# Optimization experiments

Hardware: AMD Instinct MI355X
Metric: run time of the kernel (lower is better)

Reference implementation:

```python
import jax, jax.numpy as jnp
import numpy as np


def setup_inputs() -> dict:
    key = jax.random.key(0)
    k1, k2, k3 = jax.random.split(key, 3)
    x = jax.random.normal(k1, (8, 2048, 512), dtype=jnp.float32)
    codebook = jax.random.normal(k2, (8192, 512), dtype=jnp.float32)
    values = jax.random.normal(k3, (8192, 512), dtype=jnp.float32)
    return {"x": x, "codebook": codebook, "values": values}


def reference(x, codebook, values):
    # VectorQuantize: nearest codebook entry under squared L2 distance.
    # dist(b,n,k) = ||x_bn||^2 - 2 x_bn . e_k + ||e_k||^2
    x_sq = jnp.sum(x * x, axis=-1, keepdims=True)            # [b, n, 1]
    e_sq = jnp.sum(codebook * codebook, axis=-1)             # [k]
    dots = jnp.einsum('bnd,kd->bnk', x, codebook)            # [b, n, k] (GEMM)
    memory_indices = jnp.argmin(x_sq - 2.0 * dots + e_sq, axis=-1)  # [b, n]
    # Irregular gather into the memory/value table.
    memories = values[memory_indices]                        # [b, n, dim_memory]
    return memories
```

## Files before the change

kernel.cpp:

```cpp
#include <hip/hip_runtime.h>
#include <hip/hip_bf16.h>


#define D      512
#define M      16384
#define NCODE  8192
#define NSTEP  8
#define ATILEG 131072
#define BTILEG 65536

typedef float f32x4  __attribute__((ext_vector_type(4)));
typedef short bf16x8 __attribute__((ext_vector_type(8)));

#define KMAX 0xFFFFFFFFFFFFFFFFull

__device__ __forceinline__ unsigned long long score_key(float sc, int code) {
  unsigned int u = __float_as_uint(sc);
  unsigned int su = u ^ ((unsigned int)((int)u >> 31) | 0x80000000u);
  return ((unsigned long long)su << 32) | (unsigned int)code;
}

__device__ __forceinline__ void kins2(unsigned long long k,
                                      unsigned long long& k1, unsigned long long& k2) {
  if (k < k1) { k2 = k1; k1 = k; }
  else if (k < k2) { k2 = k; }
}

__device__ __forceinline__ void kins4(unsigned long long k,
    unsigned long long& k0, unsigned long long& k1,
    unsigned long long& k2, unsigned long long& k3) {
  if (k < k0)      { k3 = k2; k2 = k1; k1 = k0; k0 = k; }
  else if (k < k1) { k3 = k2; k2 = k1; k1 = k; }
  else if (k < k2) { k3 = k2; k2 = k; }
  else if (k < k3) { k3 = k; }
}

__global__ __launch_bounds__(256)
void prep256(const float* __restrict__ src, __hip_bfloat16* __restrict__ dst) {
  __shared__ __hip_bfloat16 tile[256][72];
  const int tid = threadIdx.x;
  const int c = blockIdx.x & 7, t = blockIdx.x >> 3;
  const float* srow = src + (size_t)t * 256 * D;
  __hip_bfloat16* dbase = dst + (size_t)t * ATILEG;

#pragma unroll
  for (int j = 0; j < 8; ++j) {
    int f = tid + j * 256;
    int row = f >> 3, k16l = f & 7;
    const float4* p = (const float4*)(srow + (size_t)row * D + c * 64 + k16l * 8);
    float4 v0 = p[0], v1 = p[1];
    float vv[8] = {v0.x, v0.y, v0.z, v0.w, v1.x, v1.y, v1.z, v1.w};
    union { bf16x8 v; unsigned short u[8]; } pk;
#pragma unroll
    for (int e = 0; e < 8; ++e) {
      __hip_bfloat16 h = __float2bfloat16(vv[e]);
      pk.u[e] = *(unsigned short*)&h;
    }
    *(bf16x8*)&tile[row][k16l * 8] = pk.v;
  }
  __syncthreads();
#pragma unroll
  for (int j = 0; j < 8; ++j) {
    int g = tid + j * 256;
    int row = g & 255, k16l = g >> 8;
    bf16x8 v = *(const bf16x8*)&tile[row][k16l * 8];
    *(bf16x8*)(dbase + ((size_t)(c * 8 + k16l) * 256 + row) * 8) = v;
  }
}

__global__ __launch_bounds__(256)
void prep128(const float* __restrict__ src, __hip_bfloat16* __restrict__ dst) {
  __shared__ __hip_bfloat16 tile[128][72];
  const int tid = threadIdx.x;
  const int c = blockIdx.x & 7, t = blockIdx.x >> 3;
  const float* srow = src + (size_t)t * 128 * D;
  __hip_bfloat16* dbase = dst + (size_t)t * BTILEG;

#pragma unroll
  for (int j = 0; j < 4; ++j) {
    int f = tid + j * 256;
    int row = f >> 3, k16l = f & 7;
    const float4* p = (const float4*)(srow + (size_t)row * D + c * 64 + k16l * 8);
    float4 v0 = p[0], v1 = p[1];
    float vv[8] = {v0.x, v0.y, v0.z, v0.w, v1.x, v1.y, v1.z, v1.w};
    union { bf16x8 v; unsigned short u[8]; } pk;
#pragma unroll
    for (int e = 0; e < 8; ++e) {
      __hip_bfloat16 h = __float2bfloat16(vv[e]);
      pk.u[e] = *(unsigned short*)&h;
    }
    *(bf16x8*)&tile[row][k16l * 8] = pk.v;
  }
  __syncthreads();
#pragma unroll
  for (int j = 0; j < 4; ++j) {
    int g = tid + j * 256;
    int row = g & 127, k16l = g >> 7;
    bf16x8 v = *(const bf16x8*)&tile[row][k16l * 8];
    *(bf16x8*)(dbase + ((size_t)(c * 8 + k16l) * 128 + row) * 8) = v;
  }
}

__global__ __launch_bounds__(256)
void rowsumsq(const float* __restrict__ src, float* __restrict__ dst, int nrows) {
  int gw = (blockIdx.x * 256 + threadIdx.x) >> 6;
  if (gw >= nrows) return;
  int lane = threadIdx.x & 63;
  const float4* s4 = (const float4*)(src + (size_t)gw * D);
  float s = 0.f;
#pragma unroll
  for (int i = 0; i < 2; ++i) {
    float4 v = s4[lane + i * 64];
    s += v.x * v.x + v.y * v.y + v.z * v.z + v.w * v.w;
  }
#pragma unroll
  for (int off = 32; off > 0; off >>= 1) s += __shfl_down(s, off, 64);
  if (lane == 0) dst[gw] = s;
}

__global__ __launch_bounds__(512, 1)
void vq_gemm_rs(const __hip_bfloat16* __restrict__ Apack,
                const __hip_bfloat16* __restrict__ Bpack,
                const float* __restrict__ e_sq,
                ulonglong2* __restrict__ cand2) {
  extern __shared__ __hip_bfloat16 smem[];

  const int tid = threadIdx.x;
  const int w = tid >> 6, l = tid & 63;
  const int wr = w >> 1, wc = w & 1;
  const int lr = l & 15, lh = l >> 4;

  const int bid = blockIdx.x;
  const int xcd = bid & 7, idx = bid >> 3;
  const int mt = xcd * 8 + (idx & 7);
  const int ct = idx >> 3;

  const __hip_bfloat16* Abase = Apack + (size_t)mt * ATILEG;
  const __hip_bfloat16* Bbase = Bpack + (size_t)ct * BTILEG;

  f32x4 acc[4][4] = {};
  float4 rA[4], rB[2];

#define LOADR(t)                                                               \
  do {                                                                         \
    _Pragma("unroll")                                                          \
    for (int i = 0; i < 4; ++i)                                                \
      rA[i] = *(const float4*)(Abase + ((size_t)(t) * 2048 + tid + i * 512) * 8); \
    _Pragma("unroll")                                                          \
    for (int i = 0; i < 2; ++i)                                                \
      rB[i] = *(const float4*)(Bbase + ((size_t)(t) * 1024 + tid + i * 512) * 8); \
  } while (0)

#define WRITE(buf)                                                             \
  do {                                                                         \
    float4* Aw = (float4*)smem + (buf) * 3072;                                 \
    float4* Bw = Aw + 2048;                                                    \
    _Pragma("unroll")                                                          \
    for (int i = 0; i < 4; ++i) Aw[tid + i * 512] = rA[i];                     \
    _Pragma("unroll")                                                          \
    for (int i = 0; i < 2; ++i) Bw[tid + i * 512] = rB[i];                     \
  } while (0)

#define COMPUTE(buf)                                                           \
  do {                                                                         \
    const bf16x8* Ag = (const bf16x8*)smem + (buf) * 3072;                     \
    const bf16x8* Bg = Ag + 2048;                                              \
    _Pragma("unroll")                                                          \
    for (int kk = 0; kk < 2; ++kk) {                                           \
      const int kb = kk * 4 + lh;                                              \
      bf16x8 a[4], b[4];                                                       \
      _Pragma("unroll")                                                        \
      for (int nc = 0; nc < 4; ++nc) b[nc] = Bg[kb * 128 + wc * 64 + nc * 16 + lr]; \
      _Pragma("unroll")                                                        \
      for (int m = 0; m < 4; ++m)   a[m] = Ag[kb * 256 + wr * 64 + m * 16 + lr];    \
      _Pragma("unroll")                                                        \
      for (int nc = 0; nc < 4; ++nc)                                           \
        _Pragma("unroll")                                                      \
        for (int m = 0; m < 4; ++m)                                            \
          acc[nc][m] = __builtin_amdgcn_mfma_f32_16x16x32_bf16(b[nc], a[m],    \
                                                               acc[nc][m], 0, 0, 0); \
    }                                                                          \
  } while (0)

  LOADR(0);
  WRITE(0);
  __syncthreads();

#pragma unroll 1
  for (int t = 0; t < NSTEP - 1; ++t) {
    LOADR(t + 1);
    COMPUTE(t & 1);
    WRITE((t + 1) & 1);
    __syncthreads();
  }
  COMPUTE((NSTEP - 1) & 1);
#undef LOADR
#undef WRITE
#undef COMPUTE

  const int col0 = ct * 128 + wc * 64;
  float es[4][4];
#pragma unroll
  for (int nc = 0; nc < 4; ++nc) {
    float4 e4 = *(const float4*)&e_sq[col0 + nc * 16 + lh * 4];
    es[nc][0] = e4.x; es[nc][1] = e4.y; es[nc][2] = e4.z; es[nc][3] = e4.w;
  }
#pragma unroll
  for (int m = 0; m < 4; ++m) {
    unsigned long long k1 = KMAX, k2 = KMAX;
#pragma unroll
    for (int nc = 0; nc < 4; ++nc)
#pragma unroll
      for (int q = 0; q < 4; ++q) {
        int code = col0 + nc * 16 + lh * 4 + q;
        kins2(score_key(es[nc][q] - 2.0f * acc[nc][m][q], code), k1, k2);
      }
#pragma unroll
    for (int s = 16; s <= 32; s <<= 1) {
      unsigned long long o1 = __shfl_xor(k1, s, 64);
      unsigned long long o2 = __shfl_xor(k2, s, 64);
      kins2(o1, k1, k2);
      kins2(o2, k1, k2);
    }
    if (lh == 0) {
      int gRow = mt * 256 + wr * 64 + m * 16 + lr;
      cand2[(size_t)gRow * 128 + ct * 2 + wc] = make_ulonglong2(k1, k2);
    }
  }
}

__global__ __launch_bounds__(256)
void vq_merge4(const float* __restrict__ x, const float* __restrict__ cb,
               const float* __restrict__ values, const float* __restrict__ e_sq,
               const ulonglong2* __restrict__ cand2, float* __restrict__ out) {
  int row = blockIdx.x * 4 + (threadIdx.x >> 6);
  int l = threadIdx.x & 63;

  unsigned long long k0 = KMAX, k1 = KMAX, k2 = KMAX, k3 = KMAX;
  const ulonglong2* base = cand2 + (size_t)row * 128;
#pragma unroll
  for (int u = 0; u < 2; ++u) {
    ulonglong2 e = base[l + 64 * u];
    kins4(e.x, k0, k1, k2, k3);
    kins4(e.y, k0, k1, k2, k3);
  }
#pragma unroll
  for (int s = 1; s < 64; s <<= 1) {
    unsigned long long o0 = __shfl_xor(k0, s, 64), o1 = __shfl_xor(k1, s, 64);
    unsigned long long o2 = __shfl_xor(k2, s, 64), o3 = __shfl_xor(k3, s, 64);
    kins4(o0, k0, k1, k2, k3); kins4(o1, k0, k1, k2, k3);
    kins4(o2, k0, k1, k2, k3); kins4(o3, k0, k1, k2, k3);
  }
  int i0 = (int)(k0 & 8191), i1 = (int)(k1 & 8191);
  int i2 = (int)(k2 & 8191), i3 = (int)(k3 & 8191);

  const float4* xr = (const float4*)(x + (size_t)row * D);
  const float4* c0 = (const float4*)(cb + (size_t)i0 * D);
  const float4* c1 = (const float4*)(cb + (size_t)i1 * D);
  const float4* c2 = (const float4*)(cb + (size_t)i2 * D);
  const float4* c3 = (const float4*)(cb + (size_t)i3 * D);
  float xsq = 0.f, t0 = 0.f, t1 = 0.f, t2 = 0.f, t3 = 0.f;
#pragma unroll
  for (int u = 0; u < 2; ++u) {
    float4 xv = xr[l + 64 * u];
    float4 a = c0[l + 64 * u], b = c1[l + 64 * u];
    float4 c = c2[l + 64 * u], e = c3[l + 64 * u];
    xsq += xv.x * xv.x + xv.y * xv.y + xv.z * xv.z + xv.w * xv.w;
    t0 += xv.x * a.x + xv.y * a.y + xv.z * a.z + xv.w * a.w;
    t1 += xv.x * b.x + xv.y * b.y + xv.z * b.z + xv.w * b.w;
    t2 += xv.x * c.x + xv.y * c.y + xv.z * c.z + xv.w * c.w;
    t3 += xv.x * e.x + xv.y * e.y + xv.z * e.z + xv.w * e.w;
  }
#pragma unroll
  for (int s = 1; s < 64; s <<= 1) {
    xsq += __shfl_xor(xsq, s, 64);
    t0 += __shfl_xor(t0, s, 64); t1 += __shfl_xor(t1, s, 64);
    t2 += __shfl_xor(t2, s, 64); t3 += __shfl_xor(t3, s, 64);
  }
  float D0 = xsq - 2.0f * t0 + e_sq[i0];
  float D1 = xsq - 2.0f * t1 + e_sq[i1];
  float D2 = xsq - 2.0f * t2 + e_sq[i2];
  float D3 = xsq - 2.0f * t3 + e_sq[i3];
  float bdist = D0; int best = i0;
  if (D1 < bdist || (D1 == bdist && i1 < best)) { bdist = D1; best = i1; }
  if (D2 < bdist || (D2 == bdist && i2 < best)) { bdist = D2; best = i2; }
  if (D3 < bdist || (D3 == bdist && i3 < best)) { bdist = D3; best = i3; }

  const float4* vsrc = (const float4*)(values + (size_t)best * D);
  float4* dst = (float4*)(out + (size_t)row * D);
  dst[l] = vsrc[l];
  dst[l + 64] = vsrc[l + 64];
}

extern "C" void kernel_launch(void* const* d_in, const int* in_sizes, int n_in,
                              void* d_out, int out_size, void* d_ws, size_t ws_size,
                              hipStream_t stream) {
  const float* x      = (const float*)d_in[0];
  const float* cb     = (const float*)d_in[1];
  const float* values = (const float*)d_in[2];
  float* out = (float*)d_out;

  const size_t A_BYTES = (size_t)M * 512 * 2;
  const size_t B_BYTES = (size_t)NCODE * 512 * 2;
  const size_t C_BYTES = (size_t)M * 128 * 16;

  char* base = (char*)d_ws;
  __hip_bfloat16* Apack = (__hip_bfloat16*)base;
  __hip_bfloat16* Bpack = (__hip_bfloat16*)(base + A_BYTES);
  ulonglong2* cand2 = (ulonglong2*)(base + A_BYTES + B_BYTES);
  float* e_sq = (float*)(base + A_BYTES + B_BYTES + C_BYTES);

  const int LDS_GEMM = 98304;
  (void)hipFuncSetAttribute(reinterpret_cast<const void*>(vq_gemm_rs),
                            hipFuncAttributeMaxDynamicSharedMemorySize, LDS_GEMM);

  prep256<<<(M / 256) * 8, 256, 0, stream>>>(x, Apack);
  prep128<<<(NCODE / 128) * 8, 256, 0, stream>>>(cb, Bpack);
  rowsumsq<<<NCODE / 4, 256, 0, stream>>>(cb, e_sq, NCODE);
  vq_gemm_rs<<<(M / 256) * (NCODE / 128), 512, LDS_GEMM, stream>>>(
      Apack, Bpack, e_sq, cand2);
  vq_merge4<<<M / 4, 256, 0, stream>>>(x, cb, values, e_sq, cand2, out);
}
```

Measured before the change: 815.8 us.

## Use direct global-to-LDS loads with 256-thread blocks and two blocks per CU

Replaces the register-staged copy (global load to registers, then LDS store) with global_load_lds, so tiles go straight into shared memory. The block shrinks from 512 to 256 threads, each wave now owns 128 rows, and the launch bound allows two blocks per CU. The K step halves, giving twice as many pipeline steps with static 48KB LDS per block. The goals are to cut VGPR and LDS-store overhead and to raise occupancy for latency hiding. The risk is that each wave's 32 accumulators raise register pressure and that there are more barriers per tile.

```diff
diff --git a/kernel.cpp b/kernel.cpp
--- a/kernel.cpp
+++ b/kernel.cpp
@@ -5,7 +5,7 @@
 #define D      512
 #define M      16384
 #define NCODE  8192
-#define NSTEP  8
+#define NSTEP  16
 #define ATILEG 131072
 #define BTILEG 65536
 
@@ -13,6 +13,12 @@
 typedef short bf16x8 __attribute__((ext_vector_type(8)));
 
 #define KMAX 0xFFFFFFFFFFFFFFFFull
+
+__device__ __forceinline__ void gload16(const __hip_bfloat16* g, __hip_bfloat16* l) {
+  __builtin_amdgcn_global_load_lds(
+      (const __attribute__((address_space(1))) void*)g,
+      (__attribute__((address_space(3))) void*)l, 16, 0, 0);
+}
 
 __device__ __forceinline__ unsigned long long score_key(float sc, int code) {
   unsigned int u = __float_as_uint(sc);
@@ -118,12 +124,13 @@
   if (lane == 0) dst[gw] = s;
 }
 
-__global__ __launch_bounds__(512, 1)
-void vq_gemm_rs(const __hip_bfloat16* __restrict__ Apack,
-                const __hip_bfloat16* __restrict__ Bpack,
-                const float* __restrict__ e_sq,
-                ulonglong2* __restrict__ cand2) {
-  extern __shared__ __hip_bfloat16 smem[];
+__global__ __launch_bounds__(256, 2)
+void vq_gemm2b(const __hip_bfloat16* __restrict__ Apack,
+               const __hip_bfloat16* __restrict__ Bpack,
+               const float* __restrict__ e_sq,
+               ulonglong2* __restrict__ cand2) {
+  __shared__ __hip_bfloat16 As[2][1024 * 8];
+  __shared__ __hip_bfloat16 Bs[2][512 * 8];
 
   const int tid = threadIdx.x;
   const int w = tid >> 6, l = tid & 63;
@@ -138,64 +145,50 @@
   const __hip_bfloat16* Abase = Apack + (size_t)mt * ATILEG;
   const __hip_bfloat16* Bbase = Bpack + (size_t)ct * BTILEG;
 
-  f32x4 acc[4][4] = {};
-  float4 rA[4], rB[2];
-
-#define LOADR(t)                                                               \
+  f32x4 acc[4][8] = {};
+
+#define STAGE(buf, t)                                                          \
   do {                                                                         \
     _Pragma("unroll")                                                          \
     for (int i = 0; i < 4; ++i)                                                \
-      rA[i] = *(const float4*)(Abase + ((size_t)(t) * 2048 + tid + i * 512) * 8); \
+      gload16(Abase + ((size_t)(t) * 1024 + tid + i * 256) * 8,                \
+              As[(buf)] + (size_t)(tid + i * 256) * 8);                        \
     _Pragma("unroll")                                                          \
     for (int i = 0; i < 2; ++i)                                                \
-      rB[i] = *(const float4*)(Bbase + ((size_t)(t) * 1024 + tid + i * 512) * 8); \
-  } while (0)
-
-#define WRITE(buf)                                                             \
-  do {                                                                         \
-    float4* Aw = (float4*)smem + (buf) * 3072;                                 \
-    float4* Bw = Aw + 2048;                                                    \
-    _Pragma("unroll")                                                          \
-    for (int i = 0; i < 4; ++i) Aw[tid + i * 512] = rA[i];                     \
-    _Pragma("unroll")                                                          \
-    for (int i = 0; i < 2; ++i) Bw[tid + i * 512] = rB[i];                     \
+      gload16(Bbase + ((size_t)(t) * 512 + tid + i * 256) * 8,                 \
+              Bs[(buf)] + (size_t)(tid + i * 256) * 8);                        \
   } while (0)
 
 #define COMPUTE(buf)                                                           \
   do {                                                                         \
-    const bf16x8* Ag = (const bf16x8*)smem + (buf) * 3072;                     \
-    const bf16x8* Bg = Ag + 2048;                                              \
-    _Pragma("unroll")                                                          \
-    for (int kk = 0; kk < 2; ++kk) {                                           \
-      const int kb = kk * 4 + lh;                                              \
-      bf16x8 a[4], b[4];                                                       \
+    const bf16x8* Ag = (const bf16x8*)As[(buf)];                               \
+    const bf16x8* Bg = (const bf16x8*)Bs[(buf)];                               \
+    const int kb = lh;                                                         \
+    bf16x8 a[8], b[4];                                                         \
+    _Pragma("unroll")                                                          \
+    for (int nc = 0; nc < 4; ++nc) b[nc] = Bg[kb * 128 + wc * 64 + nc * 16 + lr]; \
+    _Pragma("unroll")                                                          \
+    for (int m = 0; m < 8; ++m)   a[m] = Ag[kb * 256 + wr * 128 + m * 16 + lr];   \
+    _Pragma("unroll")                                                          \
+    for (int nc = 0; nc < 4; ++nc)                                             \
       _Pragma("unroll")                                                        \
-      for (int nc = 0; nc < 4; ++nc) b[nc] = Bg[kb * 128 + wc * 64 + nc * 16 + lr]; \
-      _Pragma("unroll")                                                        \
-      for (int m = 0; m < 4; ++m)   a[m] = Ag[kb * 256 + wr * 64 + m * 16 + lr];    \
-      _Pragma("unroll")                                                        \
-      for (int nc = 0; nc < 4; ++nc)                                           \
-        _Pragma("unroll")                                                      \
-        for (int m = 0; m < 4; ++m)                                            \
-          acc[nc][m] = __builtin_amdgcn_mfma_f32_16x16x32_bf16(b[nc], a[m],    \
-                                                               acc[nc][m], 0, 0, 0); \
-    }                                                                          \
+      for (int m = 0; m < 8; ++m)                                              \
+        acc[nc][m] = __builtin_amdgcn_mfma_f32_16x16x32_bf16(b[nc], a[m],      \
+                                                             acc[nc][m], 0, 0, 0); \
   } while (0)
 
-  LOADR(0);
-  WRITE(0);
+  STAGE(0, 0);
   __syncthreads();
 
 #pragma unroll 1
   for (int t = 0; t < NSTEP - 1; ++t) {
-    LOADR(t + 1);
-    COMPUTE(t & 1);
-    WRITE((t + 1) & 1);
+    const int cur = t & 1;
+    STAGE(cur ^ 1, t + 1);
+    COMPUTE(cur);
     __syncthreads();
   }
   COMPUTE((NSTEP - 1) & 1);
-#undef LOADR
-#undef WRITE
+#undef STAGE
 #undef COMPUTE
 
   const int col0 = ct * 128 + wc * 64;
@@ -206,7 +199,7 @@
     es[nc][0] = e4.x; es[nc][1] = e4.y; es[nc][2] = e4.z; es[nc][3] = e4.w;
   }
 #pragma unroll
-  for (int m = 0; m < 4; ++m) {
+  for (int m = 0; m < 8; ++m) {
     unsigned long long k1 = KMAX, k2 = KMAX;
 #pragma unroll
     for (int nc = 0; nc < 4; ++nc)
@@ -223,7 +216,7 @@
       kins2(o2, k1, k2);
     }
     if (lh == 0) {
-      int gRow = mt * 256 + wr * 64 + m * 16 + lr;
+      int gRow = mt * 256 + wr * 128 + m * 16 + lr;
       cand2[(size_t)gRow * 128 + ct * 2 + wc] = make_ulonglong2(k1, k2);
     }
   }
@@ -310,14 +303,10 @@
   ulonglong2* cand2 = (ulonglong2*)(base + A_BYTES + B_BYTES);
   float* e_sq = (float*)(base + A_BYTES + B_BYTES + C_BYTES);
 
-  const int LDS_GEMM = 98304;
-  (void)hipFuncSetAttribute(reinterpret_cast<const void*>(vq_gemm_rs),
-                            hipFuncAttributeMaxDynamicSharedMemorySize, LDS_GEMM);
-
   prep256<<<(M / 256) * 8, 256, 0, stream>>>(x, Apack);
   prep128<<<(NCODE / 128) * 8, 256, 0, stream>>>(cb, Bpack);
   rowsumsq<<<NCODE / 4, 256, 0, stream>>>(cb, e_sq, NCODE);
-  vq_gemm_rs<<<(M / 256) * (NCODE / 128), 512, LDS_GEMM, stream>>>(
+  vq_gemm2b<<<(M / 256) * (NCODE / 128), 256, 0, stream>>>(
       Apack, Bpack, e_sq, cand2);
   vq_merge4<<<M / 4, 256, 0, stream>>>(x, cb, values, e_sq, cand2, out);
 }
```

Measured after the change: 798.0 us. 1.02x faster.
